# Optimization experiments

Measured on AMD Instinct MI355X. Metric: run time of the kernel, lower is better.

Reference implementation:

```python
import jax, jax.numpy as jnp
import numpy as np

COS_EPS = 1e-8   # torch F.cosine_similarity norm clamp
SIM_EPS = 1e-6   # +1e-6 added to every cosine similarity in get_cossim
LOG_EPS = 1e-6   # +1e-6 inside log in calc_loss


def setup_inputs() -> dict:
    key = jax.random.key(0)
    k1, = jax.random.split(key, 1)
    N, M, D = 1024, 16, 512
    embeddings = jax.random.normal(k1, (N, M, D), dtype=jnp.float32)
    w = jnp.asarray(10.0, dtype=jnp.float32)
    b = jnp.asarray(-5.0, dtype=jnp.float32)
    return {"embeddings": embeddings, "w": w, "b": b}


def _unit(x):
    n = jnp.sqrt(jnp.sum(x * x, axis=-1, keepdims=True))
    return x / jnp.maximum(n, COS_EPS)


def _ge2e_loss(embeddings, w, b):
    N, M, D = embeddings.shape
    e_unit = _unit(embeddings)                              # [N, M, D]

    # full centroids (mean over utterances)
    centroids = jnp.mean(embeddings, axis=1)                # [N, D]
    c_unit = _unit(centroids)                               # [N, D]

    # cosine sim of every utterance vs every speaker centroid
    cossim = jnp.einsum('nmd,kd->nmk', e_unit, c_unit)      # [N, M, N]

    # leave-one-out centroid for own-speaker entries (self-exclusion)
    loo = (jnp.sum(embeddings, axis=1, keepdims=True) - embeddings) / (M - 1)  # [N, M, D]
    diag = jnp.sum(e_unit * _unit(loo), axis=-1)            # [N, M]

    idx = jnp.arange(N)
    cossim = cossim.at[idx, :, idx].set(diag)
    cossim = cossim + SIM_EPS

    sim_matrix = w * cossim + b                             # [N, M, N]

    pos = sim_matrix[idx, :, idx]                           # [N, M]
    neg = jnp.log(jnp.sum(jnp.exp(sim_matrix), axis=2) + LOG_EPS)  # [N, M]
    return jnp.sum(neg - pos)


def reference(embeddings, w, b):
    return _ge2e_loss(embeddings, w, b)
```

## Files before the change

### kernel.cpp

```cpp
#include <hip/hip_runtime.h>

#define N_SPK 1024
#define M_UTT 16
#define D_DIM 512

typedef __attribute__((ext_vector_type(8))) short bf16x8;
typedef __attribute__((ext_vector_type(4))) float f32x4;

__device__ __forceinline__ float wave_sum64(float v) {
  #pragma unroll
  for (int off = 32; off >= 1; off >>= 1) v += __shfl_xor(v, off, 64);
  return v;
}

__device__ __forceinline__ unsigned short f2bf(float x) {
  unsigned int u = __float_as_uint(x);
  unsigned int r = (u + 0x7FFFu + ((u >> 16) & 1u)) >> 16;
  return (unsigned short)r;
}

__device__ __forceinline__ unsigned int pack_bf16(float a, float b) {
  return (unsigned int)f2bf(a) | ((unsigned int)f2bf(b) << 16);
}

__device__ __forceinline__ void gload_lds16(const void* g, void* l) {
  __builtin_amdgcn_global_load_lds(
      (const __attribute__((address_space(1))) void*)g,
      (__attribute__((address_space(3))) void*)l, 16, 0, 0);
}

__global__ __launch_bounds__(256) void prep_kernel(
    const float* __restrict__ emb, const float* __restrict__ wp,
    const float* __restrict__ bp, unsigned int* __restrict__ eU,
    unsigned int* __restrict__ cU, float* __restrict__ pos_out)
{
  const int n = blockIdx.x;
  const int t = threadIdx.x;
  __shared__ float es[M_UTT * D_DIM];
  __shared__ float Sd[D_DIM];
  __shared__ float red[4];
  __shared__ float inv_s[M_UTT];

  const float* base = emb + (size_t)n * (M_UTT * D_DIM);
  #pragma unroll
  for (int i = 0; i < 8; ++i) {
    int s = t + i * 256;
    reinterpret_cast<float4*>(es)[s] = reinterpret_cast<const float4*>(base)[s];
  }
  __syncthreads();

  #pragma unroll
  for (int rep = 0; rep < 2; ++rep) {
    int d = t + rep * 256;
    float s = 0.f;
    #pragma unroll
    for (int m = 0; m < M_UTT; ++m) s += es[m * D_DIM + d];
    Sd[d] = s;
  }
  __syncthreads();

  float p = 0.f;
  #pragma unroll
  for (int rep = 0; rep < 2; ++rep) {
    int d = t + rep * 256;
    float c = Sd[d] * (1.f / M_UTT);
    p += c * c;
  }
  p = wave_sum64(p);
  if ((t & 63) == 0) red[t >> 6] = p;
  __syncthreads();
  float cn2 = red[0] + red[1] + red[2] + red[3];
  float invc = 1.f / fmaxf(sqrtf(cn2), 1e-8f);

  {
    int d = t * 2;
    float c0 = Sd[d] * (1.f / M_UTT) * invc;
    float c1 = Sd[d + 1] * (1.f / M_UTT) * invc;
    cU[n * 256 + t] = pack_bf16(c0, c1);
  }

  const int wid = t >> 6, lane = t & 63;
  const float w = *wp, b = *bp;
  for (int m = wid; m < M_UTT; m += 4) {
    float dot = 0.f, ne = 0.f, nl = 0.f;
    #pragma unroll
    for (int r = 0; r < 8; ++r) {
      int d = lane + r * 64;
      float e = es[m * D_DIM + d];
      float l = Sd[d] - e;
      dot += e * l; ne += e * e; nl += l * l;
    }
    dot = wave_sum64(dot); ne = wave_sum64(ne); nl = wave_sum64(nl);
    if (lane == 0) {
      float inv_e = 1.f / fmaxf(sqrtf(ne), 1e-8f);
      float inv_l = 1.f / fmaxf(sqrtf(nl) * (1.f / (M_UTT - 1)), 1e-8f);
      float diag = dot * (1.f / (M_UTT - 1)) * inv_e * inv_l;
      pos_out[n * M_UTT + m] = w * (diag + 1e-6f) + b;
      inv_s[m] = inv_e;
    }
  }
  __syncthreads();

  #pragma unroll
  for (int i = 0; i < 16; ++i) {
    int p2 = t + i * 256;
    int m = p2 >> 8;
    int d = (p2 & 255) * 2;
    float sc = inv_s[m];
    float x0 = es[m * D_DIM + d] * sc;
    float x1 = es[m * D_DIM + d + 1] * sc;
    eU[(size_t)n * 4096 + p2] = pack_bf16(x0, x1);
  }
}

#define NKT 8

struct Pipe {
  const char* gA;
  const char* gB;
  char* lA;
  char* lB;
};

__device__ __forceinline__ void stage_tile(const Pipe& p, int tt) {
  const int bo = (tt & 1) << 15;
  const char* gA = p.gA + tt * 128;
  const char* gB = p.gB + tt * 128;
  gload_lds16(gA,           p.lA + bo);
  gload_lds16(gA + 65536,   p.lA + bo + 8192);
  gload_lds16(gA + 131072,  p.lA + bo + 16384);
  gload_lds16(gA + 196608,  p.lA + bo + 24576);
  gload_lds16(gB,           p.lB + bo);
  gload_lds16(gB + 65536,   p.lB + bo + 8192);
  gload_lds16(gB + 131072,  p.lB + bo + 16384);
  gload_lds16(gB + 196608,  p.lB + bo + 24576);
}

template <int MI0>
__device__ __forceinline__ void mfma_half(f32x4 acc[8][4], const bf16x8 af[4][2],
                                          const bf16x8 bf[4][2]) {
  __builtin_amdgcn_s_setprio(1);
  #pragma unroll
  for (int kk = 0; kk < 2; ++kk)
    #pragma unroll
    for (int mi = 0; mi < 4; ++mi)
      #pragma unroll
      for (int nj = 0; nj < 4; ++nj)
        acc[MI0 + mi][nj] = __builtin_amdgcn_mfma_f32_16x16x32_bf16(
            af[mi][kk], bf[nj][kk], acc[MI0 + mi][nj], 0, 0, 0);
  __builtin_amdgcn_s_setprio(0);
}

__global__ __launch_bounds__(512, 2) void mfma_kernel(
    const char* __restrict__ eU, const char* __restrict__ cU,
    const float* __restrict__ pos, const float* __restrict__ wp,
    const float* __restrict__ bp, float* __restrict__ partial)
{
  __shared__ char ldsA[65536];
  __shared__ char ldsB[65536];
  __shared__ float pos_l[256];
  __shared__ float rowsum[4][256];

  const int t = threadIdx.x;
  const int lane = t & 63;
  const int wv = t >> 6;
  const int wm = wv >> 2, wn = wv & 3;

  const int bid = blockIdx.x;
  const int sw = (bid & 7) * 32 + (bid >> 3);
  const int cb = sw & 3, rb = sw >> 2;
  const int row0 = rb * 256, col0 = cb * 256;

  const float w = *wp, b = *bp;
  const float bb = w * 1e-6f + b;

  Pipe p;
  {
    const int rowl = wv * 8 + (lane >> 3);
    const int seg = (lane & 7) ^ (lane >> 3);
    p.gA = eU + (size_t)(row0 + rowl) * 1024 + seg * 16;
    p.gB = cU + (size_t)(col0 + rowl) * 1024 + seg * 16;
    p.lA = ldsA + wv * 1024;
    p.lB = ldsB + wv * 1024;
  }

  const int j16 = lane & 15, g = lane >> 4;
  const int afb0 = (wm * 128 + j16) * 128 + (((0 * 4 + g) ^ (lane & 7)) * 16);
  const int afb1 = (wm * 128 + j16) * 128 + (((1 * 4 + g) ^ (lane & 7)) * 16);
  const int bfb0 = (wn * 64 + j16) * 128 + (((0 * 4 + g) ^ (lane & 7)) * 16);
  const int bfb1 = (wn * 64 + j16) * 128 + (((1 * 4 + g) ^ (lane & 7)) * 16);

  f32x4 acc[8][4] = {};
  bf16x8 af[4][2], bf[4][2];

  stage_tile(p, 0);

  for (int j = 0; j < NKT; ++j) {
    asm volatile("s_waitcnt vmcnt(0)" ::: "memory");
    __builtin_amdgcn_s_barrier();
    if (j < NKT - 1) stage_tile(p, j + 1);

    const int bo = (j & 1) << 15;
    #pragma unroll
    for (int nq = 0; nq < 4; ++nq) {
      bf[nq][0] = *reinterpret_cast<const bf16x8*>(ldsB + bo + bfb0 + nq * 2048);
      bf[nq][1] = *reinterpret_cast<const bf16x8*>(ldsB + bo + bfb1 + nq * 2048);
    }
    #pragma unroll
    for (int a = 0; a < 4; ++a) {
      af[a][0] = *reinterpret_cast<const bf16x8*>(ldsA + bo + afb0 + a * 2048);
      af[a][1] = *reinterpret_cast<const bf16x8*>(ldsA + bo + afb1 + a * 2048);
    }
    mfma_half<0>(acc, af, bf);
    #pragma unroll
    for (int a = 0; a < 4; ++a) {
      af[a][0] = *reinterpret_cast<const bf16x8*>(ldsA + bo + afb0 + (a + 4) * 2048);
      af[a][1] = *reinterpret_cast<const bf16x8*>(ldsA + bo + afb1 + (a + 4) * 2048);
    }
    mfma_half<4>(acc, af, bf);
  }

  if (t < 256) pos_l[t] = pos[row0 + t];
  __syncthreads();

  float esum[8][4];
  #pragma unroll
  for (int mi = 0; mi < 8; ++mi)
    #pragma unroll
    for (int rg = 0; rg < 4; ++rg) esum[mi][rg] = 0.f;

  #pragma unroll
  for (int nj = 0; nj < 4; ++nj) {
    const int kg = col0 + wn * 64 + nj * 16 + (lane & 15);
    #pragma unroll
    for (int mi = 0; mi < 8; ++mi) {
      #pragma unroll
      for (int rg = 0; rg < 4; ++rg) {
        const int r_loc = wm * 128 + mi * 16 + (lane >> 4) * 4 + rg;
        float arg = w * acc[mi][nj][rg] + bb;
        if (kg == ((row0 + r_loc) >> 4)) arg = pos_l[r_loc];
        esum[mi][rg] += __expf(arg);
      }
    }
  }
  #pragma unroll
  for (int mi = 0; mi < 8; ++mi)
    #pragma unroll
    for (int rg = 0; rg < 4; ++rg) {
      float v = esum[mi][rg];
      v += __shfl_xor(v, 1, 64);
      v += __shfl_xor(v, 2, 64);
      v += __shfl_xor(v, 4, 64);
      v += __shfl_xor(v, 8, 64);
      esum[mi][rg] = v;
    }
  if ((lane & 15) == 0) {
    #pragma unroll
    for (int mi = 0; mi < 8; ++mi)
      #pragma unroll
      for (int rg = 0; rg < 4; ++rg)
        rowsum[wn][wm * 128 + mi * 16 + (lane >> 4) * 4 + rg] = esum[mi][rg];
  }
  __syncthreads();
  if (t < 256)
    partial[(size_t)cb * (N_SPK * M_UTT) + row0 + t] =
        rowsum[0][t] + rowsum[1][t] + rowsum[2][t] + rowsum[3][t];
}

__global__ __launch_bounds__(1024) void finalize_kernel(
    const float* __restrict__ partial, const float* __restrict__ pos,
    float* __restrict__ out)
{
  const int t = threadIdx.x;
  float v = 0.f;
  #pragma unroll
  for (int i = 0; i < 16; ++i) {
    const int r = t + i * 1024;
    float s = partial[r] + partial[16384 + r] + partial[32768 + r] +
              partial[49152 + r];
    v += logf(s + 1e-6f) - pos[r];
  }
  v = wave_sum64(v);
  __shared__ float red[16];
  if ((t & 63) == 0) red[t >> 6] = v;
  __syncthreads();
  if (t == 0) {
    float s = 0.f;
    #pragma unroll
    for (int i = 0; i < 16; ++i) s += red[i];
    out[0] = s;
  }
}

extern "C" void kernel_launch(void* const* d_in, const int* in_sizes, int n_in,
                              void* d_out, int out_size, void* d_ws, size_t ws_size,
                              hipStream_t stream) {
  const float* emb = (const float*)d_in[0];
  const float* wp  = (const float*)d_in[1];
  const float* bp  = (const float*)d_in[2];
  float* out = (float*)d_out;

  char* wsb = (char*)d_ws;
  unsigned int* eU  = (unsigned int*)wsb;
  unsigned int* cU  = (unsigned int*)(wsb + 16777216);
  float* pos        = (float*)(wsb + 16777216 + 1048576);
  float* partial    = (float*)(wsb + 16777216 + 1048576 + 65536);

  prep_kernel<<<N_SPK, 256, 0, stream>>>(emb, wp, bp, eU, cU, pos);
  mfma_kernel<<<256, 512, 0, stream>>>(
      (const char*)eU, (const char*)cU, pos, wp, bp, partial);
  finalize_kernel<<<1, 1024, 0, stream>>>(partial, pos, out);
}
```

Baseline: 45.24 us.

## Switch GEMM operands to FP8 e4m3 and use scaled 32x32x64 MFMA

Quantizes the normalized utterance embeddings and centroids to FP8 e4m3 instead of bf16. This halves the intermediate buffer size and the global/LDS traffic. The GEMM now uses the MI355 scaled f8f6f4 32x32x64 MFMA with neutral scales, and the LDS tiling, swizzle and epilogue row mapping are rewritten to match. FP8 precision on the cosine similarities, multiplied by w=10 before exp, risks accuracy loss in the loss value.

```diff
diff --git a/kernel.cpp b/kernel.cpp
--- a/kernel.cpp
+++ b/kernel.cpp
@@ -1,11 +1,13 @@
 #include <hip/hip_runtime.h>
+#include <hip/hip_fp8.h>
 
 #define N_SPK 1024
 #define M_UTT 16
 #define D_DIM 512
 
-typedef __attribute__((ext_vector_type(8))) short bf16x8;
-typedef __attribute__((ext_vector_type(4))) float f32x4;
+typedef __attribute__((ext_vector_type(4))) int i32x4;
+typedef __attribute__((ext_vector_type(8))) int i32x8;
+typedef __attribute__((ext_vector_type(16))) float f32x16;
 
 __device__ __forceinline__ float wave_sum64(float v) {
   #pragma unroll
@@ -13,14 +15,13 @@
   return v;
 }
 
-__device__ __forceinline__ unsigned short f2bf(float x) {
-  unsigned int u = __float_as_uint(x);
-  unsigned int r = (u + 0x7FFFu + ((u >> 16) & 1u)) >> 16;
-  return (unsigned short)r;
-}
-
-__device__ __forceinline__ unsigned int pack_bf16(float a, float b) {
-  return (unsigned int)f2bf(a) | ((unsigned int)f2bf(b) << 16);
+__device__ __forceinline__ unsigned int pack4_e4m3(float a, float b, float c,
+                                                   float d) {
+  union { __hip_fp8_e4m3 q; unsigned char u; } A, B, C, D;
+  A.q = __hip_fp8_e4m3(a); B.q = __hip_fp8_e4m3(b);
+  C.q = __hip_fp8_e4m3(c); D.q = __hip_fp8_e4m3(d);
+  return (unsigned int)A.u | ((unsigned int)B.u << 8) |
+         ((unsigned int)C.u << 16) | ((unsigned int)D.u << 24);
 }
 
 __device__ __forceinline__ void gload_lds16(const void* g, void* l) {
@@ -72,11 +73,11 @@
   float cn2 = red[0] + red[1] + red[2] + red[3];
   float invc = 1.f / fmaxf(sqrtf(cn2), 1e-8f);
 
-  {
-    int d = t * 2;
-    float c0 = Sd[d] * (1.f / M_UTT) * invc;
-    float c1 = Sd[d + 1] * (1.f / M_UTT) * invc;
-    cU[n * 256 + t] = pack_bf16(c0, c1);
+  if (t < 128) {
+    int k0 = t * 4;
+    float sc = (1.f / M_UTT) * invc;
+    cU[n * 128 + t] = pack4_e4m3(Sd[k0] * sc, Sd[k0 + 1] * sc,
+                                 Sd[k0 + 2] * sc, Sd[k0 + 3] * sc);
   }
 
   const int wid = t >> 6, lane = t & 63;
@@ -102,62 +103,26 @@
   __syncthreads();
 
   #pragma unroll
-  for (int i = 0; i < 16; ++i) {
-    int p2 = t + i * 256;
-    int m = p2 >> 8;
-    int d = (p2 & 255) * 2;
+  for (int i = 0; i < 8; ++i) {
+    int wi = t + i * 256;
+    int m = wi >> 7;
+    int k0 = (wi & 127) * 4;
     float sc = inv_s[m];
-    float x0 = es[m * D_DIM + d] * sc;
-    float x1 = es[m * D_DIM + d + 1] * sc;
-    eU[(size_t)n * 4096 + p2] = pack_bf16(x0, x1);
+    eU[(size_t)n * 2048 + wi] =
+        pack4_e4m3(es[m * D_DIM + k0] * sc, es[m * D_DIM + k0 + 1] * sc,
+                   es[m * D_DIM + k0 + 2] * sc, es[m * D_DIM + k0 + 3] * sc);
   }
 }
 
 #define NKT 8
-
-struct Pipe {
-  const char* gA;
-  const char* gB;
-  char* lA;
-  char* lB;
-};
-
-__device__ __forceinline__ void stage_tile(const Pipe& p, int tt) {
-  const int bo = (tt & 1) << 15;
-  const char* gA = p.gA + tt * 128;
-  const char* gB = p.gB + tt * 128;
-  gload_lds16(gA,           p.lA + bo);
-  gload_lds16(gA + 65536,   p.lA + bo + 8192);
-  gload_lds16(gA + 131072,  p.lA + bo + 16384);
-  gload_lds16(gA + 196608,  p.lA + bo + 24576);
-  gload_lds16(gB,           p.lB + bo);
-  gload_lds16(gB + 65536,   p.lB + bo + 8192);
-  gload_lds16(gB + 131072,  p.lB + bo + 16384);
-  gload_lds16(gB + 196608,  p.lB + bo + 24576);
-}
-
-template <int MI0>
-__device__ __forceinline__ void mfma_half(f32x4 acc[8][4], const bf16x8 af[4][2],
-                                          const bf16x8 bf[4][2]) {
-  __builtin_amdgcn_s_setprio(1);
-  #pragma unroll
-  for (int kk = 0; kk < 2; ++kk)
-    #pragma unroll
-    for (int mi = 0; mi < 4; ++mi)
-      #pragma unroll
-      for (int nj = 0; nj < 4; ++nj)
-        acc[MI0 + mi][nj] = __builtin_amdgcn_mfma_f32_16x16x32_bf16(
-            af[mi][kk], bf[nj][kk], acc[MI0 + mi][nj], 0, 0, 0);
-  __builtin_amdgcn_s_setprio(0);
-}
 
 __global__ __launch_bounds__(512, 2) void mfma_kernel(
     const char* __restrict__ eU, const char* __restrict__ cU,
     const float* __restrict__ pos, const float* __restrict__ wp,
     const float* __restrict__ bp, float* __restrict__ partial)
 {
-  __shared__ char ldsA[65536];
-  __shared__ char ldsB[65536];
+  __shared__ char ldsA[32768];
+  __shared__ char ldsB[32768];
   __shared__ float pos_l[256];
   __shared__ float rowsum[4][256];
 
@@ -174,92 +139,106 @@
   const float w = *wp, b = *bp;
   const float bb = w * 1e-6f + b;
 
-  Pipe p;
+  unsigned int gA[2], gB[2];
+  #pragma unroll
+  for (int r = 0; r < 2; ++r) {
+    int s = t + r * 512;
+    int line = s >> 3, sp = s & 7;
+    int seg = sp ^ (line & 7);
+    int row = 2 * line + (seg >> 2);
+    int kseg = seg & 3;
+    gA[r] = (unsigned int)(row0 + row) * 512u + kseg * 16;
+    gB[r] = (unsigned int)(col0 + row) * 512u + kseg * 16;
+  }
+  char* lA = ldsA + wv * 1024;
+  char* lB = ldsB + wv * 1024;
+
+  const int rl = lane & 31, kh = lane >> 5;
+  const int seg0 = 2 * kh + 4 * (rl & 1);
+  int afb[4][2], bfb[2][2];
+  #pragma unroll
+  for (int mi = 0; mi < 4; ++mi) {
+    int line = wm * 64 + mi * 16 + (rl >> 1);
+    afb[mi][0] = line * 128 + ((seg0 ^ (line & 7)) * 16);
+    afb[mi][1] = line * 128 + (((seg0 + 1) ^ (line & 7)) * 16);
+  }
+  #pragma unroll
+  for (int nj = 0; nj < 2; ++nj) {
+    int line = wn * 32 + nj * 16 + (rl >> 1);
+    bfb[nj][0] = line * 128 + ((seg0 ^ (line & 7)) * 16);
+    bfb[nj][1] = line * 128 + (((seg0 + 1) ^ (line & 7)) * 16);
+  }
+
+  f32x16 acc[4][2] = {};
+  const int SC = 0x7F7F7F7F;
+
   {
-    const int rowl = wv * 8 + (lane >> 3);
-    const int seg = (lane & 7) ^ (lane >> 3);
-    p.gA = eU + (size_t)(row0 + rowl) * 1024 + seg * 16;
-    p.gB = cU + (size_t)(col0 + rowl) * 1024 + seg * 16;
-    p.lA = ldsA + wv * 1024;
-    p.lB = ldsB + wv * 1024;
-  }
-
-  const int j16 = lane & 15, g = lane >> 4;
-  const int afb0 = (wm * 128 + j16) * 128 + (((0 * 4 + g) ^ (lane & 7)) * 16);
-  const int afb1 = (wm * 128 + j16) * 128 + (((1 * 4 + g) ^ (lane & 7)) * 16);
-  const int bfb0 = (wn * 64 + j16) * 128 + (((0 * 4 + g) ^ (lane & 7)) * 16);
-  const int bfb1 = (wn * 64 + j16) * 128 + (((1 * 4 + g) ^ (lane & 7)) * 16);
-
-  f32x4 acc[8][4] = {};
-  bf16x8 af[4][2], bf[4][2];
-
-  stage_tile(p, 0);
+    gload_lds16(eU + gA[0], lA);
+    gload_lds16(eU + gA[1], lA + 8192);
+    gload_lds16(cU + gB[0], lB);
+    gload_lds16(cU + gB[1], lB + 8192);
+  }
 
   for (int j = 0; j < NKT; ++j) {
     asm volatile("s_waitcnt vmcnt(0)" ::: "memory");
     __builtin_amdgcn_s_barrier();
-    if (j < NKT - 1) stage_tile(p, j + 1);
-
-    const int bo = (j & 1) << 15;
-    #pragma unroll
-    for (int nq = 0; nq < 4; ++nq) {
-      bf[nq][0] = *reinterpret_cast<const bf16x8*>(ldsB + bo + bfb0 + nq * 2048);
-      bf[nq][1] = *reinterpret_cast<const bf16x8*>(ldsB + bo + bfb1 + nq * 2048);
-    }
-    #pragma unroll
-    for (int a = 0; a < 4; ++a) {
-      af[a][0] = *reinterpret_cast<const bf16x8*>(ldsA + bo + afb0 + a * 2048);
-      af[a][1] = *reinterpret_cast<const bf16x8*>(ldsA + bo + afb1 + a * 2048);
-    }
-    mfma_half<0>(acc, af, bf);
-    #pragma unroll
-    for (int a = 0; a < 4; ++a) {
-      af[a][0] = *reinterpret_cast<const bf16x8*>(ldsA + bo + afb0 + (a + 4) * 2048);
-      af[a][1] = *reinterpret_cast<const bf16x8*>(ldsA + bo + afb1 + (a + 4) * 2048);
-    }
-    mfma_half<4>(acc, af, bf);
+    if (j < NKT - 1) {
+      const int bo2 = ((j + 1) & 1) << 14;
+      const int d0 = (j + 1) * 64;
+      gload_lds16(eU + gA[0] + d0, lA + bo2);
+      gload_lds16(eU + gA[1] + d0, lA + bo2 + 8192);
+      gload_lds16(cU + gB[0] + d0, lB + bo2);
+      gload_lds16(cU + gB[1] + d0, lB + bo2 + 8192);
+    }
+
+    const int bo = (j & 1) << 14;
+    i32x8 af[4], bf[2];
+    #pragma unroll
+    for (int nj = 0; nj < 2; ++nj) {
+      i32x4 lo = *reinterpret_cast<const i32x4*>(ldsB + bo + bfb[nj][0]);
+      i32x4 hi = *reinterpret_cast<const i32x4*>(ldsB + bo + bfb[nj][1]);
+      bf[nj] = __builtin_shufflevector(lo, hi, 0, 1, 2, 3, 4, 5, 6, 7);
+    }
+    #pragma unroll
+    for (int mi = 0; mi < 4; ++mi) {
+      i32x4 lo = *reinterpret_cast<const i32x4*>(ldsA + bo + afb[mi][0]);
+      i32x4 hi = *reinterpret_cast<const i32x4*>(ldsA + bo + afb[mi][1]);
+      af[mi] = __builtin_shufflevector(lo, hi, 0, 1, 2, 3, 4, 5, 6, 7);
+    }
+    __builtin_amdgcn_s_setprio(1);
+    #pragma unroll
+    for (int mi = 0; mi < 4; ++mi)
+      #pragma unroll
+      for (int nj = 0; nj < 2; ++nj)
+        acc[mi][nj] = __builtin_amdgcn_mfma_scale_f32_32x32x64_f8f6f4(
+            af[mi], bf[nj], acc[mi][nj], 0, 0, 0, SC, 0, SC);
+    __builtin_amdgcn_s_setprio(0);
   }
 
   if (t < 256) pos_l[t] = pos[row0 + t];
   __syncthreads();
 
-  float esum[8][4];
-  #pragma unroll
-  for (int mi = 0; mi < 8; ++mi)
-    #pragma unroll
-    for (int rg = 0; rg < 4; ++rg) esum[mi][rg] = 0.f;
-
-  #pragma unroll
-  for (int nj = 0; nj < 4; ++nj) {
-    const int kg = col0 + wn * 64 + nj * 16 + (lane & 15);
-    #pragma unroll
-    for (int mi = 0; mi < 8; ++mi) {
+  #pragma unroll
+  for (int mi = 0; mi < 4; ++mi) {
+    #pragma unroll
+    for (int reg = 0; reg < 16; ++reg) {
+      const int row_loc = wm * 128 + mi * 32 + (reg & 3) + 8 * (reg >> 2) + 4 * kh;
+      const int diag_col = (row0 + row_loc) >> 4;
+      float s = 0.f;
       #pragma unroll
-      for (int rg = 0; rg < 4; ++rg) {
-        const int r_loc = wm * 128 + mi * 16 + (lane >> 4) * 4 + rg;
-        float arg = w * acc[mi][nj][rg] + bb;
-        if (kg == ((row0 + r_loc) >> 4)) arg = pos_l[r_loc];
-        esum[mi][rg] += __expf(arg);
+      for (int nj = 0; nj < 2; ++nj) {
+        const int col = col0 + wn * 64 + nj * 32 + rl;
+        float arg = w * acc[mi][nj][reg] + bb;
+        if (col == diag_col) arg = pos_l[row_loc];
+        s += __expf(arg);
       }
-    }
-  }
-  #pragma unroll
-  for (int mi = 0; mi < 8; ++mi)
-    #pragma unroll
-    for (int rg = 0; rg < 4; ++rg) {
-      float v = esum[mi][rg];
-      v += __shfl_xor(v, 1, 64);
-      v += __shfl_xor(v, 2, 64);
-      v += __shfl_xor(v, 4, 64);
-      v += __shfl_xor(v, 8, 64);
-      esum[mi][rg] = v;
-    }
-  if ((lane & 15) == 0) {
-    #pragma unroll
-    for (int mi = 0; mi < 8; ++mi)
-      #pragma unroll
-      for (int rg = 0; rg < 4; ++rg)
-        rowsum[wn][wm * 128 + mi * 16 + (lane >> 4) * 4 + rg] = esum[mi][rg];
+      s += __shfl_xor(s, 1, 64);
+      s += __shfl_xor(s, 2, 64);
+      s += __shfl_xor(s, 4, 64);
+      s += __shfl_xor(s, 8, 64);
+      s += __shfl_xor(s, 16, 64);
+      if (rl == 0) rowsum[wn][row_loc] = s;
+    }
   }
   __syncthreads();
   if (t < 256)
@@ -302,9 +281,9 @@
 
   char* wsb = (char*)d_ws;
   unsigned int* eU  = (unsigned int*)wsb;
-  unsigned int* cU  = (unsigned int*)(wsb + 16777216);
-  float* pos        = (float*)(wsb + 16777216 + 1048576);
-  float* partial    = (float*)(wsb + 16777216 + 1048576 + 65536);
+  unsigned int* cU  = (unsigned int*)(wsb + 8388608);
+  float* pos        = (float*)(wsb + 8388608 + 524288);
+  float* partial    = (float*)(wsb + 8388608 + 524288 + 65536);
 
   prep_kernel<<<N_SPK, 256, 0, stream>>>(emb, wp, bp, eU, cU, pos);
   mfma_kernel<<<256, 512, 0, stream>>>(
```

After: 67.71 us. 49.7% more time.
